# Kernel tuning notes

Hardware: AMD Instinct MI355X
Metric: run time of the kernel (lower is better)

The kernel has to match this reference:

```python
import jax, jax.numpy as jnp
import numpy as np

INPUT_DIM, HIDDEN_DIM, OUTPUT_DIM = 64, 256, 64
# AutoNCP(256, 64): inter_and_command=192, command=int(0.4*192)=76, inter=116, motor=64
INTER, COMMAND, MOTOR = 116, 76, 64
SENSORY_FANOUT, INTER_FANOUT, MOTOR_FANIN = 58, 38, 38
B, T = 512, 256


def setup_inputs() -> dict:
    rng = np.random.default_rng(0)
    key = jax.random.key(0)
    d = {}
    # NCP wiring sparsity (binary masks; ncps takes abs() so polarity is irrelevant for the mask)
    m0 = np.zeros((INTER, INPUT_DIM), np.float32)
    for i in range(INPUT_DIM):
        m0[rng.choice(INTER, SENSORY_FANOUT, replace=False), i] = 1.0
    m1 = np.zeros((COMMAND, INTER), np.float32)
    for i in range(INTER):
        m1[rng.choice(COMMAND, INTER_FANOUT, replace=False), i] = 1.0
    m2 = np.zeros((MOTOR, COMMAND), np.float32)
    for o in range(MOTOR):
        m2[o, rng.choice(COMMAND, MOTOR_FANIN, replace=False)] = 1.0
    dims = [(INPUT_DIM, INTER, m0), (INTER, COMMAND, m1), (COMMAND, MOTOR, m2)]
    for l, (fi, h, m) in enumerate(dims):
        cat = fi + h
        # mask shape [h, fi+h]: sparse prev-layer block + all-ones recurrent block (as in WiredCfCCell)
        d[f"mask_{l}"] = jnp.asarray(np.concatenate([m, np.ones((h, h), np.float32)], axis=1))
        bound = float(1.0 / np.sqrt(cat))
        for nm in ("ff1", "ff2", "ta", "tb"):
            key, k1, k2 = jax.random.split(key, 3)
            d[f"w_{nm}_{l}"] = jax.random.uniform(k1, (h, cat), minval=-bound, maxval=bound, dtype=jnp.float32)
            d[f"b_{nm}_{l}"] = jax.random.uniform(k2, (h,), minval=-bound, maxval=bound, dtype=jnp.float32)
    key, k1, k2, kx = jax.random.split(key, 4)
    bound = float(1.0 / np.sqrt(OUTPUT_DIM))
    d["w_fc"] = jax.random.uniform(k1, (OUTPUT_DIM, OUTPUT_DIM), minval=-bound, maxval=bound, dtype=jnp.float32)
    d["b_fc"] = jax.random.uniform(k2, (OUTPUT_DIM,), minval=-bound, maxval=bound, dtype=jnp.float32)
    d["x"] = jax.random.normal(kx, (B, T, INPUT_DIM), dtype=jnp.float32)
    return d


def _cfc_cell(xin, h, w1, b1, w2, b2, wa, ba, wb, bb, mask):
    # CfCCell 'default' mode, no backbone, ts = 1.0
    cat = jnp.concatenate([xin, h], axis=-1)          # [B, fi+h]
    ff1 = jnp.tanh(cat @ (w1 * mask).T + b1)
    ff2 = jnp.tanh(cat @ (w2 * mask).T + b2)
    t_interp = jax.nn.sigmoid(cat @ wa.T + ba + cat @ wb.T + bb)  # sigmoid(t_a*1.0 + t_b)
    return ff1 * (1.0 - t_interp) + t_interp * ff2


def _forward(x, layer_params, masks, w_fc, b_fc):
    bsz = x.shape[0]
    h0 = tuple(jnp.zeros((bsz, h), x.dtype) for h in (INTER, COMMAND, MOTOR))

    def step(hs, xt):
        inp = xt
        new = []
        for l in range(3):  # inter -> command -> motor (structurally distinct layers)
            h = _cfc_cell(inp, hs[l], *layer_params[l], masks[l])
            inp = h
            new.append(h)
        return tuple(new), inp  # motor-layer output per step

    _, ys = jax.lax.scan(step, h0, jnp.swapaxes(x, 0, 1))
    y = jnp.swapaxes(ys, 0, 1)  # [B, T, MOTOR]
    return y @ w_fc.T + b_fc


def reference(x, w_ff1_0, b_ff1_0, w_ff2_0, b_ff2_0, w_ta_0, b_ta_0, w_tb_0, b_tb_0,
              w_ff1_1, b_ff1_1, w_ff2_1, b_ff2_1, w_ta_1, b_ta_1, w_tb_1, b_tb_1,
              w_ff1_2, b_ff1_2, w_ff2_2, b_ff2_2, w_ta_2, b_ta_2, w_tb_2, b_tb_2,
              w_fc, b_fc, mask_0, mask_1, mask_2):
    layer_params = [
        (w_ff1_0, b_ff1_0, w_ff2_0, b_ff2_0, w_ta_0, b_ta_0, w_tb_0, b_tb_0),
        (w_ff1_1, b_ff1_1, w_ff2_1, b_ff2_1, w_ta_1, b_ta_1, w_tb_1, b_tb_1),
        (w_ff1_2, b_ff1_2, w_ff2_2, b_ff2_2, w_ta_2, b_ta_2, w_tb_2, b_tb_2),
    ]
    return _forward(x, layer_params, (mask_0, mask_1, mask_2), w_fc, b_fc)
```

## Files before the change

### kernel.cpp

```cpp
#include <hip/hip_runtime.h>

typedef _Float16 f16x8 __attribute__((ext_vector_type(8)));
typedef _Float16 f16x4 __attribute__((ext_vector_type(4)));
typedef _Float16 f16x2 __attribute__((ext_vector_type(2)));
typedef float f32x4 __attribute__((ext_vector_type(4)));

#define NTH 1024
#define SEQT 256
#define LD0 200
#define LD1 200
#define LD2 168

struct KArgs { const float* in[30]; float* out; };

__device__ __forceinline__ float fast_tanh(float x) {
  return __fdividef(2.0f, 1.0f + __expf(-2.0f * x)) - 1.0f;
}
__device__ __forceinline__ float fast_sig(float x) {
  return __fdividef(1.0f, 1.0f + __expf(-x));
}

__device__ __forceinline__ f32x4 mfma16(f16x8 a, f16x8 b, f32x4 c) {
  return __builtin_amdgcn_mfma_f32_16x16x32_f16(a, b, c, 0, 0, 0);
}

__device__ __forceinline__ f16x4 combine3(const f32x4 acc[3]) {
  f16x4 v;
  #pragma unroll
  for (int q = 0; q < 4; ++q) {
    const float ff1 = fast_tanh(acc[0][q]);
    const float ff2 = fast_tanh(acc[1][q]);
    const float ti  = fast_sig(acc[2][q]);
    v[q] = (_Float16)(ff1 + ti * (ff2 - ff1));
  }
  return v;
}

template<int KT>
__device__ __forceinline__ void load_tile(f16x8* wW, const float* W1, const float* W2,
                                          const float* Wa, const float* Wb,
                                          const float* Mk, int n, int CAT, int H, int kb) {
  #pragma unroll
  for (int kt = 0; kt < KT; ++kt) {
    #pragma unroll
    for (int m = 0; m < 3; ++m) {
      f16x8 f;
      #pragma unroll
      for (int j = 0; j < 8; ++j) {
        const int k = kt * 32 + kb + j;
        float v = 0.f;
        if (n < H && k < CAT) {
          if (m == 0)      v = W1[n*CAT+k] * Mk[n*CAT+k];
          else if (m == 1) v = W2[n*CAT+k] * Mk[n*CAT+k];
          else             v = Wa[n*CAT+k] + Wb[n*CAT+k];
        }
        f[j] = (_Float16)v;
      }
      wW[m*KT + kt] = f;
    }
  }
}

template<int KT>
__device__ __forceinline__ void mma_tile_ld(f32x4 acc[3], const f16x8* wW,
                                            const _Float16* __restrict__ c,
                                            int LD, int r, int kb) {
  #pragma unroll
  for (int kt = 0; kt < KT; ++kt) {
    const f16x8 b = *reinterpret_cast<const f16x8*>(c + r*LD + kt*32 + kb);
    #pragma unroll
    for (int m = 0; m < 3; ++m)
      acc[m] = mfma16(wW[m*KT + kt], b, acc[m]);
  }
}

__device__ __forceinline__ void init3(f32x4 acc[3], const float* sb, int bs, int n0) {
  #pragma unroll
  for (int m = 0; m < 3; ++m)
    acc[m] = *reinterpret_cast<const f32x4*>(sb + m*bs + n0);
}

__device__ __forceinline__ f16x8 loadB8u(const _Float16* p) {
  const f16x4 a = *reinterpret_cast<const f16x4*>(p);
  const f16x4 b = *reinterpret_cast<const f16x4*>(p + 4);
  f16x8 v;
  v[0]=a[0]; v[1]=a[1]; v[2]=a[2]; v[3]=a[3];
  v[4]=b[0]; v[5]=b[1]; v[6]=b[2]; v[7]=b[3];
  return v;
}

__global__ __launch_bounds__(NTH, 4) void ncp_fused(KArgs args) {
  __shared__ __align__(16) _Float16 c0[2][16 * LD0];
  __shared__ __align__(16) _Float16 c1[2][16 * LD1];
  __shared__ __align__(16) _Float16 c2[2][16 * LD2];
  __shared__ __align__(16) _Float16 wt3[15 * 64 * 8];
  __shared__ __align__(16) _Float16 wfcs[8 * 64 * 8];
  __shared__ float b0s[3 * 128], b1s[3 * 80], b2s[3 * 64], bfcs[64];

  const int tid  = threadIdx.x;
  const int wv   = tid >> 6;
  const int lane = tid & 63;
  const int r    = lane & 15;
  const int g    = lane >> 4;
  const int kb   = g * 8;
  const int wgBase = blockIdx.x * 16;
  const float* __restrict__ xg = args.in[29];

  f16x8 wW[18];
  if (wv < 8) {
    load_tile<6>(wW, args.in[1], args.in[3], args.in[5], args.in[7], args.in[0],
                 wv*16 + r, 180, 116, kb);
  } else if (wv < 13) {
    load_tile<6>(wW, args.in[10], args.in[12], args.in[14], args.in[16], args.in[9],
                 (wv-8)*16 + r, 192, 76, kb);
  } else {
    load_tile<5>(wW, args.in[19], args.in[21], args.in[23], args.in[25], args.in[18],
                 (wv-13)*16 + r, 140, 64, kb);
  }

  for (int u = tid; u < 15 * 64; u += NTH) {
    const int ln = u & 63;
    const int ff = u >> 6;
    const int kt = ff % 5, m = ff / 5;
    const int n  = 48 + (ln & 15);
    const int kbb = (ln >> 4) * 8;
    f16x8 f;
    #pragma unroll
    for (int j = 0; j < 8; ++j) {
      const int k = kt*32 + kbb + j;
      float v = 0.f;
      if (k < 140) {
        if (m == 0)      v = args.in[19][n*140+k] * args.in[18][n*140+k];
        else if (m == 1) v = args.in[21][n*140+k] * args.in[18][n*140+k];
        else             v = args.in[23][n*140+k] + args.in[25][n*140+k];
      }
      f[j] = (_Float16)v;
    }
    *reinterpret_cast<f16x8*>(wt3 + (size_t)u * 8) = f;
  }
  for (int u = tid; u < 8 * 64; u += NTH) {
    const int ln = u & 63;
    const int ff = u >> 6;
    const int kt = ff & 1, ot = ff >> 1;
    f16x8 f;
    #pragma unroll
    for (int j = 0; j < 8; ++j)
      f[j] = (_Float16)args.in[27][(ot*16 + (ln & 15))*64 + kt*32 + (ln >> 4)*8 + j];
    *reinterpret_cast<f16x8*>(wfcs + (size_t)u * 8) = f;
  }
  if (tid < 128) {
    b0s[tid]       = (tid < 116) ? args.in[2][tid] : 0.f;
    b0s[128 + tid] = (tid < 116) ? args.in[4][tid] : 0.f;
    b0s[256 + tid] = (tid < 116) ? args.in[6][tid] + args.in[8][tid] : 0.f;
  }
  if (tid < 80) {
    b1s[tid]       = (tid < 76) ? args.in[11][tid] : 0.f;
    b1s[80 + tid]  = (tid < 76) ? args.in[13][tid] : 0.f;
    b1s[160 + tid] = (tid < 76) ? args.in[15][tid] + args.in[17][tid] : 0.f;
  }
  if (tid < 64) {
    b2s[tid]       = args.in[20][tid];
    b2s[64 + tid]  = args.in[22][tid];
    b2s[128 + tid] = args.in[24][tid] + args.in[26][tid];
    bfcs[tid]      = args.in[28][tid];
  }
  for (int i = tid; i < 2 * 16 * LD0; i += NTH) c0[0][i] = (_Float16)0.f;
  for (int i = tid; i < 2 * 16 * LD1; i += NTH) c1[0][i] = (_Float16)0.f;
  for (int i = tid; i < 2 * 16 * LD2; i += NTH) c2[0][i] = (_Float16)0.f;
  __syncthreads();
  const int rr = (tid & 511) >> 5, cc = (tid & 31) * 2;
  if (tid < 512) {
    const float2 v = *reinterpret_cast<const float2*>(
        xg + ((size_t)(wgBase + rr) * SEQT) * 64 + cc);
    f16x2 pk; pk[0] = (_Float16)v.x; pk[1] = (_Float16)v.y;
    *reinterpret_cast<f16x2*>(c0[0] + rr * LD0 + cc) = pk;
  }
  __syncthreads();

  const float* xp = xg + ((size_t)(wgBase + rr) * SEQT + 1) * 64 + cc;
  const int otb = (wv >= 13) ? (wv - 13) : 0;
  float* outp = args.out + ((size_t)(wgBase + r) * SEQT) * 64 + otb * 32 + 4 * g;

  #pragma unroll 1
  for (int p = 0; p < SEQT + 3; ++p) {
    const int cur = p & 1, nxt = cur ^ 1;

    float2 xv;
    const bool doX = (tid < 512) && (p < SEQT - 1);
    if (doX) xv = *reinterpret_cast<const float2*>(xp);

    if (wv < 8) {
      if (p < SEQT) {
        f32x4 a[3];
        const int nb = wv*16 + 4*g;
        init3(a, b0s, 128, nb);
        __builtin_amdgcn_s_setprio(1);
        mma_tile_ld<6>(a, wW, c0[cur], LD0, r, kb);
        __builtin_amdgcn_s_setprio(0);
        const f16x4 v = combine3(a);
        if (nb < 116) {
          *reinterpret_cast<f16x4*>(c1[nxt] + r*LD1 + nb)      = v;
          *reinterpret_cast<f16x4*>(c0[nxt] + r*LD0 + 64 + nb) = v;
        }
      }
    } else if (wv < 13) {
      if (p >= 1 && p <= SEQT) {
        f32x4 a[3];
        const int nb = (wv-8)*16 + 4*g;
        init3(a, b1s, 80, nb);
        __builtin_amdgcn_s_setprio(1);
        mma_tile_ld<6>(a, wW, c1[cur], LD1, r, kb);
        __builtin_amdgcn_s_setprio(0);
        const f16x4 v = combine3(a);
        if (nb < 76) {
          *reinterpret_cast<f16x4*>(c1[nxt] + r*LD1 + 116 + nb) = v;
          *reinterpret_cast<f16x4*>(c2[nxt] + r*LD2 + nb)       = v;
        }
      }
    } else if (wv < 15) {
      if (p >= 3) {
        const int ot0 = (wv - 13) * 2;
        f32x4 fa0 = *reinterpret_cast<const f32x4*>(bfcs + ot0*16 + 4*g);
        f32x4 fa1 = *reinterpret_cast<const f32x4*>(bfcs + ot0*16 + 16 + 4*g);
        const f16x8 hb0 = loadB8u(c2[cur] + r*LD2 + 76 + kb);
        const f16x8 hb1 = loadB8u(c2[cur] + r*LD2 + 76 + 32 + kb);
        const f16x8 wf00 = *reinterpret_cast<const f16x8*>(wfcs + (size_t)((ot0*2    )*64 + lane)*8);
        const f16x8 wf01 = *reinterpret_cast<const f16x8*>(wfcs + (size_t)((ot0*2 + 1)*64 + lane)*8);
        const f16x8 wf10 = *reinterpret_cast<const f16x8*>(wfcs + (size_t)((ot0*2 + 2)*64 + lane)*8);
        const f16x8 wf11 = *reinterpret_cast<const f16x8*>(wfcs + (size_t)((ot0*2 + 3)*64 + lane)*8);
        fa0 = mfma16(wf00, hb0, fa0); fa0 = mfma16(wf01, hb1, fa0);
        fa1 = mfma16(wf10, hb0, fa1); fa1 = mfma16(wf11, hb1, fa1);
        *reinterpret_cast<f32x4*>(outp)      = fa0;
        *reinterpret_cast<f32x4*>(outp + 16) = fa1;
        outp += 64;
      }
      if (p >= 2 && p <= SEQT + 1) {
        f32x4 a[3];
        const int nb = (wv-13)*16 + 4*g;
        init3(a, b2s, 64, nb);
        __builtin_amdgcn_s_setprio(1);
        mma_tile_ld<5>(a, wW, c2[cur], LD2, r, kb);
        __builtin_amdgcn_s_setprio(0);
        const f16x4 v = combine3(a);
        *reinterpret_cast<f16x4*>(c2[nxt] + r*LD2 + 76 + nb) = v;
      }
    } else {
      if (p >= 2 && p <= SEQT + 1) {
        f32x4 a2[3], a3[3];
        init3(a2, b2s, 64, 32 + 4*g);
        init3(a3, b2s, 64, 48 + 4*g);
        __builtin_amdgcn_s_setprio(1);
        #pragma unroll
        for (int kt = 0; kt < 5; ++kt) {
          const f16x8 b = *reinterpret_cast<const f16x8*>(c2[cur] + r*LD2 + kt*32 + kb);
          #pragma unroll
          for (int m = 0; m < 3; ++m) {
            a2[m] = mfma16(wW[m*5 + kt], b, a2[m]);
            const f16x8 af = *reinterpret_cast<const f16x8*>(
                wt3 + (size_t)((m*5 + kt)*64 + lane) * 8);
            a3[m] = mfma16(af, b, a3[m]);
          }
        }
        __builtin_amdgcn_s_setprio(0);
        const f16x4 v2 = combine3(a2);
        const f16x4 v3 = combine3(a3);
        *reinterpret_cast<f16x4*>(c2[nxt] + r*LD2 + 76 + 32 + 4*g) = v2;
        *reinterpret_cast<f16x4*>(c2[nxt] + r*LD2 + 76 + 48 + 4*g) = v3;
      }
    }

    if (doX) {
      f16x2 pk; pk[0] = (_Float16)xv.x; pk[1] = (_Float16)xv.y;
      *reinterpret_cast<f16x2*>(c0[nxt] + rr * LD0 + cc) = pk;
      xp += 64;
    }
    __syncthreads();
  }
}

extern "C" void kernel_launch(void* const* d_in, const int* in_sizes, int n_in,
                              void* d_out, int out_size, void* d_ws, size_t ws_size,
                              hipStream_t stream) {
  KArgs args;
  for (int i = 0; i < 30; ++i) args.in[i] = (const float*)d_in[i];
  args.out = (float*)d_out;
  ncp_fused<<<dim3(32), dim3(NTH), 0, stream>>>(args);
}
```

Measured before the change: 712.7 us.

## Load x directly into MFMA B-registers per wave and streamline activations

Each layer-0 wave now loads its own slice of the input x from global memory straight into registers as packed f16 MFMA operands. This replaces staging x through the shared-memory c0 buffer. It prefetches the next timestep during the current MFMA work, and the old global-load, convert and LDS-store path before the barrier is removed. The activation math now uses exp2 with pre-scaled constants and packed round-toward-zero f16 conversion, which adds redundant global x loads across the eight layer-0 waves and slightly different rounding.

Measured after the change: 926.5 us. +30.0%, slower.

```diff
diff --git a/kernel.cpp b/kernel.cpp
--- a/kernel.cpp
+++ b/kernel.cpp
@@ -13,26 +13,37 @@
 
 struct KArgs { const float* in[30]; float* out; };
 
-__device__ __forceinline__ float fast_tanh(float x) {
-  return __fdividef(2.0f, 1.0f + __expf(-2.0f * x)) - 1.0f;
-}
-__device__ __forceinline__ float fast_sig(float x) {
-  return __fdividef(1.0f, 1.0f + __expf(-x));
-}
-
 __device__ __forceinline__ f32x4 mfma16(f16x8 a, f16x8 b, f32x4 c) {
   return __builtin_amdgcn_mfma_f32_16x16x32_f16(a, b, c, 0, 0, 0);
 }
 
-__device__ __forceinline__ f16x4 combine3(const f32x4 acc[3]) {
-  f16x4 v;
+__device__ __forceinline__ f16x2 cvt_pk(float x, float y) {
+  return __builtin_bit_cast(f16x2, __builtin_amdgcn_cvt_pkrtz(x, y));
+}
+
+__device__ __forceinline__ f16x4 combine_pack(const f32x4 a[3]) {
+  float h[4];
   #pragma unroll
   for (int q = 0; q < 4; ++q) {
-    const float ff1 = fast_tanh(acc[0][q]);
-    const float ff2 = fast_tanh(acc[1][q]);
-    const float ti  = fast_sig(acc[2][q]);
-    v[q] = (_Float16)(ff1 + ti * (ff2 - ff1));
-  }
+    const float ff1 = 1.0f - __fdividef(2.0f, 1.0f + __builtin_amdgcn_exp2f(2.885390082f * a[0][q]));
+    const float ff2 = 1.0f - __fdividef(2.0f, 1.0f + __builtin_amdgcn_exp2f(2.885390082f * a[1][q]));
+    const float ti  = __fdividef(1.0f, 1.0f + __builtin_amdgcn_exp2f(-1.442695041f * a[2][q]));
+    h[q] = ff1 + ti * (ff2 - ff1);
+  }
+  const f16x2 lo = cvt_pk(h[0], h[1]);
+  const f16x2 hi = cvt_pk(h[2], h[3]);
+  f16x4 v; v[0]=lo[0]; v[1]=lo[1]; v[2]=hi[0]; v[3]=hi[1];
+  return v;
+}
+
+__device__ __forceinline__ f16x8 pack8(const float4 v0, const float4 v1) {
+  const f16x2 a = cvt_pk(v0.x, v0.y);
+  const f16x2 b = cvt_pk(v0.z, v0.w);
+  const f16x2 c = cvt_pk(v1.x, v1.y);
+  const f16x2 d = cvt_pk(v1.z, v1.w);
+  f16x8 v;
+  v[0]=a[0]; v[1]=a[1]; v[2]=b[0]; v[3]=b[1];
+  v[4]=c[0]; v[5]=c[1]; v[6]=d[0]; v[7]=d[1];
   return v;
 }
 
@@ -61,19 +72,6 @@
   }
 }
 
-template<int KT>
-__device__ __forceinline__ void mma_tile_ld(f32x4 acc[3], const f16x8* wW,
-                                            const _Float16* __restrict__ c,
-                                            int LD, int r, int kb) {
-  #pragma unroll
-  for (int kt = 0; kt < KT; ++kt) {
-    const f16x8 b = *reinterpret_cast<const f16x8*>(c + r*LD + kt*32 + kb);
-    #pragma unroll
-    for (int m = 0; m < 3; ++m)
-      acc[m] = mfma16(wW[m*KT + kt], b, acc[m]);
-  }
-}
-
 __device__ __forceinline__ void init3(f32x4 acc[3], const float* sb, int bs, int n0) {
   #pragma unroll
   for (int m = 0; m < 3; ++m)
@@ -103,6 +101,7 @@
   const int r    = lane & 15;
   const int g    = lane >> 4;
   const int kb   = g * 8;
+  const int n4g  = 4 * g;
   const int wgBase = blockIdx.x * 16;
   const float* __restrict__ xg = args.in[29];
 
@@ -168,66 +167,93 @@
   for (int i = tid; i < 2 * 16 * LD1; i += NTH) c1[0][i] = (_Float16)0.f;
   for (int i = tid; i < 2 * 16 * LD2; i += NTH) c2[0][i] = (_Float16)0.f;
   __syncthreads();
-  const int rr = (tid & 511) >> 5, cc = (tid & 31) * 2;
-  if (tid < 512) {
-    const float2 v = *reinterpret_cast<const float2*>(
-        xg + ((size_t)(wgBase + rr) * SEQT) * 64 + cc);
-    f16x2 pk; pk[0] = (_Float16)v.x; pk[1] = (_Float16)v.y;
-    *reinterpret_cast<f16x2*>(c0[0] + rr * LD0 + cc) = pk;
-  }
-  __syncthreads();
-
-  const float* xp = xg + ((size_t)(wgBase + rr) * SEQT + 1) * 64 + cc;
+
+  const float* xq = xg + ((size_t)(wgBase + r) * SEQT) * 64 + kb;
+  f16x8 xA0, xA1;
+  if (wv < 8) {
+    const float4 a0 = *reinterpret_cast<const float4*>(xq);
+    const float4 a1 = *reinterpret_cast<const float4*>(xq + 4);
+    const float4 a2 = *reinterpret_cast<const float4*>(xq + 32);
+    const float4 a3 = *reinterpret_cast<const float4*>(xq + 36);
+    xA0 = pack8(a0, a1);
+    xA1 = pack8(a2, a3);
+  }
+  xq += 64;
+
+  const int nb0 = wv*16 + n4g;
+  const int nb1 = (wv-8)*16 + n4g;
+  const int nb2 = (wv-13)*16 + n4g;
   const int otb = (wv >= 13) ? (wv - 13) : 0;
-  float* outp = args.out + ((size_t)(wgBase + r) * SEQT) * 64 + otb * 32 + 4 * g;
+  float* outp = args.out + ((size_t)(wgBase + r) * SEQT) * 64 + otb * 32 + n4g;
 
   #pragma unroll 1
   for (int p = 0; p < SEQT + 3; ++p) {
     const int cur = p & 1, nxt = cur ^ 1;
 
-    float2 xv;
-    const bool doX = (tid < 512) && (p < SEQT - 1);
-    if (doX) xv = *reinterpret_cast<const float2*>(xp);
-
     if (wv < 8) {
       if (p < SEQT) {
+        float4 q0, q1, q2, q3;
+        const bool ldx = (p < SEQT - 1);
+        if (ldx) {
+          q0 = *reinterpret_cast<const float4*>(xq);
+          q1 = *reinterpret_cast<const float4*>(xq + 4);
+          q2 = *reinterpret_cast<const float4*>(xq + 32);
+          q3 = *reinterpret_cast<const float4*>(xq + 36);
+        }
         f32x4 a[3];
-        const int nb = wv*16 + 4*g;
-        init3(a, b0s, 128, nb);
+        init3(a, b0s, 128, nb0);
         __builtin_amdgcn_s_setprio(1);
-        mma_tile_ld<6>(a, wW, c0[cur], LD0, r, kb);
+        #pragma unroll
+        for (int m = 0; m < 3; ++m) a[m] = mfma16(wW[m*6 + 0], xA0, a[m]);
+        #pragma unroll
+        for (int m = 0; m < 3; ++m) a[m] = mfma16(wW[m*6 + 1], xA1, a[m]);
+        #pragma unroll
+        for (int kt = 2; kt < 6; ++kt) {
+          const f16x8 b = *reinterpret_cast<const f16x8*>(&c0[cur][r*LD0 + kt*32 + kb]);
+          #pragma unroll
+          for (int m = 0; m < 3; ++m) a[m] = mfma16(wW[m*6 + kt], b, a[m]);
+        }
         __builtin_amdgcn_s_setprio(0);
-        const f16x4 v = combine3(a);
-        if (nb < 116) {
-          *reinterpret_cast<f16x4*>(c1[nxt] + r*LD1 + nb)      = v;
-          *reinterpret_cast<f16x4*>(c0[nxt] + r*LD0 + 64 + nb) = v;
+        const f16x4 v = combine_pack(a);
+        if (nb0 < 116) {
+          *reinterpret_cast<f16x4*>(&c1[nxt][r*LD1 + nb0])      = v;
+          *reinterpret_cast<f16x4*>(&c0[nxt][r*LD0 + 64 + nb0]) = v;
+        }
+        if (ldx) {
+          xA0 = pack8(q0, q1);
+          xA1 = pack8(q2, q3);
+          xq += 64;
         }
       }
     } else if (wv < 13) {
       if (p >= 1 && p <= SEQT) {
         f32x4 a[3];
-        const int nb = (wv-8)*16 + 4*g;
-        init3(a, b1s, 80, nb);
+        init3(a, b1s, 80, nb1);
         __builtin_amdgcn_s_setprio(1);
-        mma_tile_ld<6>(a, wW, c1[cur], LD1, r, kb);
+        #pragma unroll
+        for (int kt = 0; kt < 6; ++kt) {
+          const f16x8 b = *reinterpret_cast<const f16x8*>(&c1[cur][r*LD1 + kt*32 + kb]);
+          #pragma unroll
+          for (int m = 0; m < 3; ++m) a[m] = mfma16(wW[m*6 + kt], b, a[m]);
+        }
         __builtin_amdgcn_s_setprio(0);
-        const f16x4 v = combine3(a);
-        if (nb < 76) {
-          *reinterpret_cast<f16x4*>(c1[nxt] + r*LD1 + 116 + nb) = v;
-          *reinterpret_cast<f16x4*>(c2[nxt] + r*LD2 + nb)       = v;
+        const f16x4 v = combine_pack(a);
+        if (nb1 < 76) {
+          *reinterpret_cast<f16x4*>(&c1[nxt][r*LD1 + 116 + nb1]) = v;
+          *reinterpret_cast<f16x4*>(&c2[nxt][r*LD2 + nb1])       = v;
         }
       }
     } else if (wv < 15) {
       if (p >= 3) {
         const int ot0 = (wv - 13) * 2;
-        f32x4 fa0 = *reinterpret_cast<const f32x4*>(bfcs + ot0*16 + 4*g);
-        f32x4 fa1 = *reinterpret_cast<const f32x4*>(bfcs + ot0*16 + 16 + 4*g);
-        const f16x8 hb0 = loadB8u(c2[cur] + r*LD2 + 76 + kb);
-        const f16x8 hb1 = loadB8u(c2[cur] + r*LD2 + 76 + 32 + kb);
-        const f16x8 wf00 = *reinterpret_cast<const f16x8*>(wfcs + (size_t)((ot0*2    )*64 + lane)*8);
-        const f16x8 wf01 = *reinterpret_cast<const f16x8*>(wfcs + (size_t)((ot0*2 + 1)*64 + lane)*8);
-        const f16x8 wf10 = *reinterpret_cast<const f16x8*>(wfcs + (size_t)((ot0*2 + 2)*64 + lane)*8);
-        const f16x8 wf11 = *reinterpret_cast<const f16x8*>(wfcs + (size_t)((ot0*2 + 3)*64 + lane)*8);
+        f32x4 fa0 = *reinterpret_cast<const f32x4*>(bfcs + ot0*16 + n4g);
+        f32x4 fa1 = *reinterpret_cast<const f32x4*>(bfcs + ot0*16 + 16 + n4g);
+        const f16x8 hb0 = loadB8u(&c2[cur][r*LD2 + 76 + kb]);
+        const f16x8 hb1 = loadB8u(&c2[cur][r*LD2 + 76 + 32 + kb]);
+        const f16x8 wf00 = *reinterpret_cast<const f16x8*>(&wfcs[((size_t)((ot0*2    )*64 + lane))*8]);
+        const f16x8 wf01 = *reinterpret_cast<const f16x8*>(&wfcs[((size_t)((ot0*2 + 1)*64 + lane))*8]);
+        const f16x8 wf10 = *reinterpret_cast<const f16x8*>(&wfcs[((size_t)((ot0*2 + 2)*64 + lane))*8]);
+        const f16x8 wf11 = *reinterpret_cast<const f16x8*>(&wfcs[((size_t)((ot0*2 + 3)*64 + lane))*8]);
         fa0 = mfma16(wf00, hb0, fa0); fa0 = mfma16(wf01, hb1, fa0);
         fa1 = mfma16(wf10, hb0, fa1); fa1 = mfma16(wf11, hb1, fa1);
         *reinterpret_cast<f32x4*>(outp)      = fa0;
@@ -236,44 +262,42 @@
       }
       if (p >= 2 && p <= SEQT + 1) {
         f32x4 a[3];
-        const int nb = (wv-13)*16 + 4*g;
-        init3(a, b2s, 64, nb);
+        init3(a, b2s, 64, nb2);
         __builtin_amdgcn_s_setprio(1);
-        mma_tile_ld<5>(a, wW, c2[cur], LD2, r, kb);
+        #pragma unroll
+        for (int kt = 0; kt < 5; ++kt) {
+          const f16x8 b = *reinterpret_cast<const f16x8*>(&c2[cur][r*LD2 + kt*32 + kb]);
+          #pragma unroll
+          for (int m = 0; m < 3; ++m) a[m] = mfma16(wW[m*5 + kt], b, a[m]);
+        }
         __builtin_amdgcn_s_setprio(0);
-        const f16x4 v = combine3(a);
-        *reinterpret_cast<f16x4*>(c2[nxt] + r*LD2 + 76 + nb) = v;
+        const f16x4 v = combine_pack(a);
+        *reinterpret_cast<f16x4*>(&c2[nxt][r*LD2 + 76 + nb2]) = v;
       }
     } else {
       if (p >= 2 && p <= SEQT + 1) {
         f32x4 a2[3], a3[3];
-        init3(a2, b2s, 64, 32 + 4*g);
-        init3(a3, b2s, 64, 48 + 4*g);
+        init3(a2, b2s, 64, 32 + n4g);
+        init3(a3, b2s, 64, 48 + n4g);
         __builtin_amdgcn_s_setprio(1);
         #pragma unroll
         for (int kt = 0; kt < 5; ++kt) {
-          const f16x8 b = *reinterpret_cast<const f16x8*>(c2[cur] + r*LD2 + kt*32 + kb);
+          const f16x8 b = *reinterpret_cast<const f16x8*>(&c2[cur][r*LD2 + kt*32 + kb]);
           #pragma unroll
           for (int m = 0; m < 3; ++m) {
             a2[m] = mfma16(wW[m*5 + kt], b, a2[m]);
-            const f16x8 af = *reinterpret_cast<const f16x8*>(
-                wt3 + (size_t)((m*5 + kt)*64 + lane) * 8);
+            const f16x8 af = *reinterpret_cast<const f16x8*>(&wt3[((size_t)((m*5 + kt)*64 + lane))*8]);
             a3[m] = mfma16(af, b, a3[m]);
           }
         }
         __builtin_amdgcn_s_setprio(0);
-        const f16x4 v2 = combine3(a2);
-        const f16x4 v3 = combine3(a3);
-        *reinterpret_cast<f16x4*>(c2[nxt] + r*LD2 + 76 + 32 + 4*g) = v2;
-        *reinterpret_cast<f16x4*>(c2[nxt] + r*LD2 + 76 + 48 + 4*g) = v3;
+        const f16x4 v2 = combine_pack(a2);
+        const f16x4 v3 = combine_pack(a3);
+        *reinterpret_cast<f16x4*>(&c2[nxt][r*LD2 + 76 + 32 + n4g]) = v2;
+        *reinterpret_cast<f16x4*>(&c2[nxt][r*LD2 + 76 + 48 + n4g]) = v3;
       }
     }
 
-    if (doX) {
-      f16x2 pk; pk[0] = (_Float16)xv.x; pk[1] = (_Float16)xv.y;
-      *reinterpret_cast<f16x2*>(c0[nxt] + rr * LD0 + cc) = pk;
-      xp += 64;
-    }
     __syncthreads();
   }
 }
```
